# Kernel optimization log

Measured on AMD Instinct MI355X. Metric: run time of the kernel, lower is better.

Reference implementation:

```python
import jax, jax.numpy as jnp
import numpy as np


def _proj(x, w, b):
    # 1x1 conv as channel matmul: x (n,c,h,w), w (k,c), b (k,) -> (n,k,h,w)
    return jnp.einsum('nchw,kc->nkhw', x, w) + b[None, :, None, None]


def setup_inputs() -> dict:
    key = jax.random.key(0)
    ks = jax.random.split(key, 9)
    cin, cinter = 256, 128
    n, h, w = 4, 64, 64
    s = lambda fan_in: 1.0 / np.sqrt(fan_in)
    return {
        'x': jax.random.normal(ks[0], (n, cin, h, w), jnp.float32),
        'theta_w': jax.random.normal(ks[1], (cinter, cin), jnp.float32) * s(cin),
        'theta_b': jax.random.normal(ks[2], (cinter,), jnp.float32) * 0.01,
        'phi_w': jax.random.normal(ks[3], (cinter, cin), jnp.float32) * s(cin),
        'phi_b': jax.random.normal(ks[4], (cinter,), jnp.float32) * 0.01,
        'g_w': jax.random.normal(ks[5], (cinter, cin), jnp.float32) * s(cin),
        'g_b': jax.random.normal(ks[6], (cinter,), jnp.float32) * 0.01,
        'w_w': jax.random.normal(ks[7], (cin, cinter), jnp.float32) * s(cinter),
        'w_b': jax.random.normal(ks[8], (cin,), jnp.float32) * 0.01,
    }


def reference(x, theta_w, theta_b, phi_w, phi_b, g_w, g_b, w_w, w_b):
    n, c, h, w = x.shape
    cinter = theta_w.shape[0]
    hw = h * w
    theta_x = _proj(x, theta_w, theta_b).reshape(n, cinter, hw)  # (n,ci,HW)
    phi_x = _proj(x, phi_w, phi_b).reshape(n, cinter, hw)        # (n,ci,HW)
    g_x = _proj(x, g_w, g_b).reshape(n, cinter, hw)              # (n,ci,HW)
    # f_x = phi^T @ theta : (n, HW, HW), softmax over last dim (theta positions)
    f_x = jnp.einsum('nci,ncj->nij', phi_x, theta_x)
    f_x = jax.nn.softmax(f_x, axis=-1)
    # attended = g @ f : (n, ci, HW)
    att = jnp.einsum('nci,nij->ncj', g_x, f_x).reshape(n, cinter, h, w)
    res_x = _proj(att, w_w, w_b)  # (n, c, h, w)
    return x + res_x
```

## Files before the change

kernel.cpp:

```cpp
#include <hip/hip_runtime.h>
#include <hip/hip_bf16.h>

#define B_ 4
#define C_ 256
#define CI_ 128
#define P_ 4096
#define LOG2E 1.44269504088896340736f

typedef __attribute__((ext_vector_type(8))) _Float16 half8;
typedef __attribute__((ext_vector_type(2))) __fp16 fp16x2;
typedef __attribute__((ext_vector_type(8))) short short8;
typedef __attribute__((ext_vector_type(4))) short short4v;
typedef __attribute__((ext_vector_type(4))) float floatx4;

__device__ __forceinline__ float bf2f(ushort h) {
  union { unsigned u; float f; } v; v.u = ((unsigned)h) << 16; return v.f;
}
__device__ __forceinline__ ushort f2bf(float f) {
  union { float f; unsigned u; } v; v.f = f;
  unsigned r = v.u + 0x7FFFu + ((v.u >> 16) & 1u);
  return (ushort)(r >> 16);
}
__device__ __forceinline__ ushort f2h(float f) {
  _Float16 h = (_Float16)f;
  union { _Float16 h; ushort u; } v; v.h = h; return v.u;
}
__device__ __forceinline__ uint2 pk4h(float a, float b, float c, float d) {
  union { fp16x2 h[2]; uint2 u; } pk;
  pk.h[0] = __builtin_amdgcn_cvt_pkrtz(a, b);
  pk.h[1] = __builtin_amdgcn_cvt_pkrtz(c, d);
  return pk.u;
}

#define MFMA16(a, b, c) __builtin_amdgcn_mfma_f32_16x16x32_f16((a), (b), (c), 0, 0, 0)

__device__ __forceinline__ int detect_bf16(const ushort* __restrict__ xu) {
  __shared__ int cnt_;
  if (threadIdx.x == 0) cnt_ = 0;
  __syncthreads();
  int local = 0;
  int t = threadIdx.x & 255;
#pragma unroll
  for (int s = 0; s < 8; ++s) {
    ushort u = xu[(t * 8 + s) * 2];
    int e = (u >> 7) & 0xFF;
    local += (e >= 0x70 && e <= 0x84) ? 1 : 0;
  }
  atomicAdd(&cnt_, local);
  __syncthreads();
  return cnt_ > 1024;
}

__global__ void k_trc(const void* __restrict__ xv, ushort* __restrict__ xT,
                      const void* __restrict__ s0, const void* __restrict__ s1,
                      const void* __restrict__ s2, const void* __restrict__ s3,
                      const void* __restrict__ tbv, const void* __restrict__ pbv,
                      const void* __restrict__ gbv, const void* __restrict__ wbv,
                      ushort* __restrict__ dstW, float* __restrict__ biasf) {
  int is_bf16 = detect_bf16((const ushort*)xv);
  int bid = blockIdx.x;
  int t = threadIdx.x;
  if (bid < 1024) {
    __shared__ __align__(16) ushort tile[64][72];
    int pb = (bid & 63) * 64;
    int cb = ((bid >> 6) & 3) * 64;
    int b = bid >> 8;
#pragma unroll
    for (int it = 0; it < 2; ++it) {
      int lin = it * 256 + t;
      int c = lin >> 3;
      int p = (lin & 7) * 8;
      size_t base = ((size_t)(b * C_) + cb + c) * P_ + pb + p;
      float vv[8];
      if (is_bf16) {
        short8 v = *(const short8*)((const ushort*)xv + base);
#pragma unroll
        for (int i = 0; i < 8; ++i) vv[i] = bf2f((ushort)v[i]);
      } else {
        const float* xf = (const float*)xv;
        float4 v0 = *(const float4*)(xf + base);
        float4 v1 = *(const float4*)(xf + base + 4);
        vv[0] = v0.x; vv[1] = v0.y; vv[2] = v0.z; vv[3] = v0.w;
        vv[4] = v1.x; vv[5] = v1.y; vv[6] = v1.z; vv[7] = v1.w;
      }
#pragma unroll
      for (int i = 0; i < 8; ++i) {
        int iw = (i + t) & 7;
        tile[p + iw][c] = f2h(vv[iw]);
      }
    }
    __syncthreads();
#pragma unroll
    for (int it = 0; it < 2; ++it) {
      int lin = it * 256 + t;
      int p = lin >> 3;
      int c = (lin & 7) * 8;
      short8 v = *(const short8*)&tile[p][c];
      *(short8*)(xT + ((size_t)(b * P_) + pb + p) * C_ + cb + c) = v;
    }
  } else if (bid < 1536) {
    int wid = bid - 1024;
    int a = wid >> 7;
    const void* srcs[4] = {s0, s1, s2, s3};
    int i = (wid & 127) * 256 + t;
    float v = is_bf16 ? bf2f(((const ushort*)srcs[a])[i]) : ((const float*)srcs[a])[i];
    dstW[a * 32768 + i] = f2h(v);
  } else {
    int idx = (bid - 1536) * 256 + t;
    if (idx < 640) {
      const void* src; int loc;
      if (idx < 128)      { src = tbv; loc = idx; }
      else if (idx < 256) { src = pbv; loc = idx - 128; }
      else if (idx < 384) { src = gbv; loc = idx - 256; }
      else                { src = wbv; loc = idx - 384; }
      float v = is_bf16 ? bf2f(((const ushort*)src)[loc]) : ((const float*)src)[loc];
      biasf[idx] = v;
    }
  }
}

__global__ __launch_bounds__(256, 4) void k_proj(
    const ushort* __restrict__ xT, const ushort* __restrict__ Wh,
    const float* __restrict__ biasf,
    ushort* __restrict__ thetaT, ushort* __restrict__ phiT,
    ushort* __restrict__ g) {
  int t = threadIdx.x;
  int w = t >> 6, lane = t & 63, l = lane & 15, q = lane >> 4;
  int pblk = blockIdx.x * 32;
  int b = blockIdx.y;
  floatx4 acc[2][6];
#pragma unroll
  for (int ps = 0; ps < 2; ++ps)
#pragma unroll
    for (int ks = 0; ks < 6; ++ks) acc[ps][ks] = (floatx4){0.f, 0.f, 0.f, 0.f};
  const ushort* xrow[2];
#pragma unroll
  for (int ps = 0; ps < 2; ++ps)
    xrow[ps] = xT + ((size_t)(b * P_) + pblk + ps * 16 + l) * C_;
  const ushort* wrow[6];
  int prj[6], kloc[6];
#pragma unroll
  for (int ks = 0; ks < 6; ++ks) {
    int kg = w * 96 + ks * 16;
    prj[ks] = kg >> 7;
    kloc[ks] = kg & 127;
    wrow[ks] = Wh + prj[ks] * 32768 + (size_t)(kloc[ks] + l) * C_;
  }
  for (int c = 0; c < C_; c += 32) {
    half8 av[2], wv[6];
#pragma unroll
    for (int ps = 0; ps < 2; ++ps) av[ps] = *(const half8*)(xrow[ps] + c + q * 8);
#pragma unroll
    for (int ks = 0; ks < 6; ++ks) wv[ks] = *(const half8*)(wrow[ks] + c + q * 8);
#pragma unroll
    for (int ps = 0; ps < 2; ++ps)
#pragma unroll
      for (int ks = 0; ks < 6; ++ks)
        acc[ps][ks] = MFMA16(av[ps], wv[ks], acc[ps][ks]);
  }
#pragma unroll
  for (int ks = 0; ks < 6; ++ks) {
    float bias = biasf[prj[ks] * 128 + kloc[ks] + l];
#pragma unroll
    for (int ps = 0; ps < 2; ++ps) {
      floatx4 d = acc[ps][ks];
      if (prj[ks] < 2) {
        ushort* dst = (prj[ks] == 0 ? thetaT : phiT) +
                      ((size_t)(b * P_) + pblk + ps * 16 + q * 4) * CI_ + kloc[ks] + l;
#pragma unroll
        for (int r = 0; r < 4; ++r) dst[(size_t)r * CI_] = f2h(d[r] + bias);
      } else {
        ushort* dst = g + ((size_t)(b * CI_) + kloc[ks] + l) * P_ + pblk + ps * 16 + q * 4;
        short4v pk;
#pragma unroll
        for (int r = 0; r < 4; ++r) pk[r] = (short)f2h(d[r] + bias);
        *(short4v*)dst = pk;
      }
    }
  }
}

__global__ __launch_bounds__(256, 2) void k_stats(
    const ushort* __restrict__ phiT, const ushort* __restrict__ thetaT,
    float* __restrict__ part) {
  int t = threadIdx.x, w = t >> 6, lane = t & 63, l = lane & 15, q = lane >> 4;
  int i0 = blockIdx.x * 256, j0 = blockIdx.y * 512, b = blockIdx.z;
  half8 av[4][4];
#pragma unroll
  for (int is = 0; is < 4; ++is) {
    const ushort* pr = phiT + ((size_t)(b * P_) + i0 + w * 64 + is * 16 + l) * CI_;
#pragma unroll
    for (int ks = 0; ks < 4; ++ks) av[is][ks] = *(const half8*)(pr + ks * 32 + q * 8);
  }
  float sum[4][4];
#pragma unroll
  for (int is = 0; is < 4; ++is)
#pragma unroll
    for (int r = 0; r < 4; ++r) sum[is][r] = 0.f;
  const ushort* tb0 = thetaT + (size_t)b * P_ * CI_;
  for (int jc = 0; jc < 16; ++jc) {
    int j = j0 + jc * 32;
    half8 bv[2][4];
#pragma unroll
    for (int js = 0; js < 2; ++js) {
      const ushort* tr = tb0 + (size_t)(j + js * 16 + l) * CI_;
#pragma unroll
      for (int ks = 0; ks < 4; ++ks) bv[js][ks] = *(const half8*)(tr + ks * 32 + q * 8);
    }
    floatx4 accS[4][2];
#pragma unroll
    for (int is = 0; is < 4; ++is)
#pragma unroll
      for (int js = 0; js < 2; ++js) accS[is][js] = (floatx4){0.f, 0.f, 0.f, 0.f};
#pragma unroll
    for (int ks = 0; ks < 4; ++ks)
#pragma unroll
      for (int is = 0; is < 4; ++is)
#pragma unroll
        for (int js = 0; js < 2; ++js)
          accS[is][js] = MFMA16(av[is][ks], bv[js][ks], accS[is][js]);
#pragma unroll
    for (int is = 0; is < 4; ++is)
#pragma unroll
      for (int js = 0; js < 2; ++js)
#pragma unroll
        for (int r = 0; r < 4; ++r)
          sum[is][r] += exp2f(fmaf(accS[is][js][r], LOG2E, -64.f));
  }
#pragma unroll
  for (int d = 1; d < 16; d <<= 1)
#pragma unroll
    for (int is = 0; is < 4; ++is)
#pragma unroll
      for (int r = 0; r < 4; ++r) sum[is][r] += __shfl_xor(sum[is][r], d, 64);
  if (l == 0) {
#pragma unroll
    for (int is = 0; is < 4; ++is)
#pragma unroll
      for (int r = 0; r < 4; ++r)
        part[((size_t)blockIdx.y * B_ + b) * P_ + i0 + w * 64 + is * 16 + q * 4 + r] =
            sum[is][r];
  }
}

__global__ void k_lse(const float* __restrict__ part, float* __restrict__ o2) {
  int idx = blockIdx.x * 256 + threadIdx.x;
  float s = 0.f;
#pragma unroll
  for (int p = 0; p < 8; ++p) s += part[(size_t)p * (B_ * P_) + idx];
  o2[idx] = log2f(s) + 64.f;
}

__global__ __launch_bounds__(256, 2) void k_attn(
    const ushort* __restrict__ phiT, const ushort* __restrict__ thetaT,
    const ushort* __restrict__ g, const float* __restrict__ o2,
    ushort* __restrict__ attPA, ushort* __restrict__ attPB, int nChunk) {
  __shared__ __align__(16) ushort thL[128][136];
  __shared__ __align__(16) ushort eL[128][136];
  int t = threadIdx.x;
  int w = t >> 6, lane = t & 63, l = lane & 15, q = lane >> 4;
  int j0 = blockIdx.x * 128, ih = blockIdx.y, b = blockIdx.z;
#pragma unroll
  for (int it = 0; it < 8; ++it) {
    int lin = it * 256 + t, row = lin >> 4, cg = (lin & 15) * 8;
    *(short8*)&thL[row][cg] =
        *(const short8*)(thetaT + ((size_t)(b * P_) + j0 + row) * CI_ + cg);
  }
  floatx4 accA[2][8];
#pragma unroll
  for (int cs = 0; cs < 2; ++cs)
#pragma unroll
    for (int js = 0; js < 8; ++js) accA[cs][js] = (floatx4){0.f, 0.f, 0.f, 0.f};
  __syncthreads();
  const float* orow = o2 + b * P_;
  int istart = ih * nChunk * 128;
  half8 af[2][4];
  float ov[2][4];
#pragma unroll
  for (int is = 0; is < 2; ++is) {
    int iG = istart + w * 32 + is * 16;
    const ushort* pr = phiT + ((size_t)(b * P_) + iG + l) * CI_;
#pragma unroll
    for (int ks = 0; ks < 4; ++ks) af[is][ks] = *(const half8*)(pr + ks * 32 + q * 8);
#pragma unroll
    for (int r = 0; r < 4; ++r) ov[is][r] = orow[iG + q * 4 + r];
  }
  for (int ic = 0; ic < nChunk; ++ic) {
    int ibase = istart + ic * 128;
    half8 gf[2][4];
#pragma unroll
    for (int cs = 0; cs < 2; ++cs) {
      const ushort* gr = g + ((size_t)(b * CI_) + w * 32 + cs * 16 + l) * P_ + ibase;
#pragma unroll
      for (int ks = 0; ks < 4; ++ks) gf[cs][ks] = *(const half8*)(gr + ks * 32 + q * 8);
    }
    floatx4 accS[2][8];
#pragma unroll
    for (int is = 0; is < 2; ++is)
#pragma unroll
      for (int js = 0; js < 8; ++js) accS[is][js] = (floatx4){0.f, 0.f, 0.f, 0.f};
#pragma unroll
    for (int ks = 0; ks < 4; ++ks) {
      half8 bf[8];
#pragma unroll
      for (int js = 0; js < 8; ++js) bf[js] = *(const half8*)&thL[js * 16 + l][ks * 32 + q * 8];
#pragma unroll
      for (int is = 0; is < 2; ++is)
#pragma unroll
        for (int js = 0; js < 8; ++js) accS[is][js] = MFMA16(af[is][ks], bf[js], accS[is][js]);
    }
    uint2 ep[2][8];
#pragma unroll
    for (int is = 0; is < 2; ++is)
#pragma unroll
      for (int js = 0; js < 8; ++js) {
        float e0 = exp2f(fmaf(accS[is][js][0], LOG2E, -ov[is][0]));
        float e1 = exp2f(fmaf(accS[is][js][1], LOG2E, -ov[is][1]));
        float e2 = exp2f(fmaf(accS[is][js][2], LOG2E, -ov[is][2]));
        float e3 = exp2f(fmaf(accS[is][js][3], LOG2E, -ov[is][3]));
        ep[is][js] = pk4h(e0, e1, e2, e3);
      }
    __syncthreads();
#pragma unroll
    for (int is = 0; is < 2; ++is)
#pragma unroll
      for (int js = 0; js < 8; ++js)
        *(uint2*)&eL[js * 16 + l][w * 32 + is * 16 + q * 4] = ep[is][js];
    __syncthreads();
    if (ic < nChunk - 1) {
      int nb = istart + (ic + 1) * 128;
#pragma unroll
      for (int is = 0; is < 2; ++is) {
        int iG = nb + w * 32 + is * 16;
        const ushort* pr = phiT + ((size_t)(b * P_) + iG + l) * CI_;
#pragma unroll
        for (int ks = 0; ks < 4; ++ks) af[is][ks] = *(const half8*)(pr + ks * 32 + q * 8);
#pragma unroll
        for (int r = 0; r < 4; ++r) ov[is][r] = orow[iG + q * 4 + r];
      }
    }
#pragma unroll
    for (int ks = 0; ks < 4; ++ks) {
      half8 ef[8];
#pragma unroll
      for (int js = 0; js < 8; ++js) ef[js] = *(const half8*)&eL[js * 16 + l][ks * 32 + q * 8];
#pragma unroll
      for (int cs = 0; cs < 2; ++cs)
#pragma unroll
        for (int js = 0; js < 8; ++js) accA[cs][js] = MFMA16(gf[cs][ks], ef[js], accA[cs][js]);
    }
  }
  ushort* ap = (ih < 2 ? attPA : attPB) + (size_t)(ih & 1) * (B_ * P_ * CI_);
#pragma unroll
  for (int cs = 0; cs < 2; ++cs)
#pragma unroll
    for (int js = 0; js < 8; ++js) {
      uint2 pk = pk4h(accA[cs][js][0], accA[cs][js][1], accA[cs][js][2], accA[cs][js][3]);
      *(uint2*)(ap + ((size_t)(b * P_) + j0 + js * 16 + l) * CI_ +
                w * 32 + cs * 16 + q * 4) = pk;
    }
}

__global__ __launch_bounds__(256, 4) void k_out(
    const ushort* __restrict__ attPA, const ushort* __restrict__ attPB, int nIH,
    const ushort* __restrict__ wwh, const float* __restrict__ biasf,
    const void* __restrict__ xv, void* __restrict__ outv) {
  int is_bf16 = detect_bf16((const ushort*)xv);
  int t = threadIdx.x;
  int w = t >> 6, lane = t & 63, l = lane & 15, q = lane >> 4;
  int p0 = blockIdx.x * 32, b = blockIdx.y;
  floatx4 accR[4][2];
#pragma unroll
  for (int kk = 0; kk < 4; ++kk)
#pragma unroll
    for (int js = 0; js < 2; ++js) accR[kk][js] = (floatx4){0.f, 0.f, 0.f, 0.f};
#pragma unroll
  for (int ks = 0; ks < 4; ++ks) {
    half8 wf[4], af[2];
#pragma unroll
    for (int kk = 0; kk < 4; ++kk)
      wf[kk] = *(const half8*)(wwh + (size_t)(w * 64 + kk * 16 + l) * CI_ + ks * 32 + q * 8);
#pragma unroll
    for (int js = 0; js < 2; ++js) {
      size_t off = ((size_t)(b * P_) + p0 + js * 16 + l) * CI_ + ks * 32 + q * 8;
      half8 s = *(const half8*)(attPA + off);
      s = s + *(const half8*)(attPA + (size_t)(B_ * P_) * CI_ + off);
      if (nIH == 4) {
        s = s + *(const half8*)(attPB + off);
        s = s + *(const half8*)(attPB + (size_t)(B_ * P_) * CI_ + off);
      }
      af[js] = s;
    }
#pragma unroll
    for (int kk = 0; kk < 4; ++kk)
#pragma unroll
      for (int js = 0; js < 2; ++js) accR[kk][js] = MFMA16(wf[kk], af[js], accR[kk][js]);
  }
#pragma unroll
  for (int kk = 0; kk < 4; ++kk)
#pragma unroll
    for (int r = 0; r < 4; ++r) {
      int c = w * 64 + kk * 16 + q * 4 + r;
      float bias = biasf[384 + c];
#pragma unroll
      for (int js = 0; js < 2; ++js) {
        int p = p0 + js * 16 + l;
        size_t idx = ((size_t)(b * C_) + c) * P_ + p;
        float val = accR[kk][js][r] + bias;
        if (is_bf16) {
          ((ushort*)outv)[idx] = f2bf(bf2f(((const ushort*)xv)[idx]) + val);
        } else {
          ((float*)outv)[idx] = ((const float*)xv)[idx] + val;
        }
      }
    }
}

extern "C" void kernel_launch(void* const* d_in, const int* in_sizes, int n_in,
                              void* d_out, int out_size, void* d_ws, size_t ws_size,
                              hipStream_t stream) {
  const void* x  = d_in[0];
  const void* tw = d_in[1];
  const void* tb = d_in[2];
  const void* pw = d_in[3];
  const void* pb = d_in[4];
  const void* gw = d_in[5];
  const void* gb = d_in[6];
  const void* ww = d_in[7];
  const void* wb = d_in[8];
  char* ws = (char*)d_ws;
  float*  o2     = (float*)(ws);
  float*  part   = (float*)(ws + (64u << 10));
  ushort* Wh     = (ushort*)(ws + (576u << 10));
  float*  biasf  = (float*)(ws + (832u << 10));
  ushort* xT     = (ushort*)(ws + (1u << 20));
  ushort* attPA  = xT;
  ushort* thetaT = (ushort*)(ws + (9u << 20));
  ushort* phiT   = (ushort*)(ws + (13u << 20));
  ushort* gbuf   = (ushort*)(ws + (17u << 20));
  ushort* attPB  = (ushort*)(ws + (21u << 20));
  int big = (ws_size >= (30u << 20)) ? 1 : 0;

  k_trc<<<1539, 256, 0, stream>>>(x, xT, tw, pw, gw, ww, tb, pb, gb, wb, Wh, biasf);
  k_proj<<<dim3(128, 4), 256, 0, stream>>>(xT, Wh, biasf, thetaT, phiT, gbuf);
  k_stats<<<dim3(16, 8, 4), 256, 0, stream>>>(phiT, thetaT, part);
  k_lse<<<64, 256, 0, stream>>>(part, o2);
  if (big) {
    k_attn<<<dim3(32, 4, 4), 256, 0, stream>>>(phiT, thetaT, gbuf, o2, attPA, attPB, 8);
    k_out<<<dim3(128, 4), 256, 0, stream>>>(attPA, attPB, 4, Wh + 3 * 32768, biasf, x, d_out);
  } else {
    k_attn<<<dim3(32, 2, 4), 256, 0, stream>>>(phiT, thetaT, gbuf, o2, attPA, attPB, 16);
    k_out<<<dim3(128, 4), 256, 0, stream>>>(attPA, attPB, 2, Wh + 3 * 32768, biasf, x, d_out);
  }
}
```

Before: 235.0 us.

## Restructure attention kernel with 32x32 MFMA, register-resident probabilities and per-wave row splits

Rewrites k_attn to use 32x32x16 MFMA tiles with a 64-column block. Each wave processes its own 32-row slices of the i dimension, and the exp'd probabilities are rearranged into the B-operand layout via cross-half-wave shuffles instead of round-tripping through LDS with two barriers per chunk. Per-wave partial accumulators are reduced through shared memory at the end in fp16, and the grid is fixed at two i-halves, so k_out sums only two partial buffers. Exp arguments are also clamped at 8. The aim is to remove LDS traffic and synchronization from the inner loop and to increase MFMA efficiency. The cost is a larger shared reduction buffer, fp16 rounding of partial sums, and reading g directly from global memory per wave.

Result: slower. 259.9 us (+10.6%).

```diff
diff --git a/kernel.cpp b/kernel.cpp
--- a/kernel.cpp
+++ b/kernel.cpp
@@ -12,6 +12,7 @@
 typedef __attribute__((ext_vector_type(8))) short short8;
 typedef __attribute__((ext_vector_type(4))) short short4v;
 typedef __attribute__((ext_vector_type(4))) float floatx4;
+typedef __attribute__((ext_vector_type(16))) float floatx16;
 
 __device__ __forceinline__ float bf2f(ushort h) {
   union { unsigned u; float f; } v; v.u = ((unsigned)h) << 16; return v.f;
@@ -25,14 +26,14 @@
   _Float16 h = (_Float16)f;
   union { _Float16 h; ushort u; } v; v.h = h; return v.u;
 }
-__device__ __forceinline__ uint2 pk4h(float a, float b, float c, float d) {
-  union { fp16x2 h[2]; uint2 u; } pk;
-  pk.h[0] = __builtin_amdgcn_cvt_pkrtz(a, b);
-  pk.h[1] = __builtin_amdgcn_cvt_pkrtz(c, d);
-  return pk.u;
+__device__ __forceinline__ uint pk2h(float a, float b) {
+  union { fp16x2 h2; uint u; } cv;
+  cv.h2 = __builtin_amdgcn_cvt_pkrtz(a, b);
+  return cv.u;
 }
 
 #define MFMA16(a, b, c) __builtin_amdgcn_mfma_f32_16x16x32_f16((a), (b), (c), 0, 0, 0)
+#define MFMA32(a, b, c) __builtin_amdgcn_mfma_f32_32x32x16_f16((a), (b), (c), 0, 0, 0)
 
 __device__ __forceinline__ int detect_bf16(const ushort* __restrict__ xu) {
   __shared__ int cnt_;
@@ -254,115 +255,131 @@
 __global__ __launch_bounds__(256, 2) void k_attn(
     const ushort* __restrict__ phiT, const ushort* __restrict__ thetaT,
     const ushort* __restrict__ g, const float* __restrict__ o2,
-    ushort* __restrict__ attPA, ushort* __restrict__ attPB, int nChunk) {
-  __shared__ __align__(16) ushort thL[128][136];
-  __shared__ __align__(16) ushort eL[128][136];
+    ushort* __restrict__ attP0, ushort* __restrict__ attP1) {
+  __shared__ __align__(16) ushort thL[64 * 136];
+  __shared__ __align__(16) uint redbuf[3 * 4096];
   int t = threadIdx.x;
-  int w = t >> 6, lane = t & 63, l = lane & 15, q = lane >> 4;
-  int j0 = blockIdx.x * 128, ih = blockIdx.y, b = blockIdx.z;
-#pragma unroll
-  for (int it = 0; it < 8; ++it) {
-    int lin = it * 256 + t, row = lin >> 4, cg = (lin & 15) * 8;
-    *(short8*)&thL[row][cg] =
-        *(const short8*)(thetaT + ((size_t)(b * P_) + j0 + row) * CI_ + cg);
-  }
-  floatx4 accA[2][8];
-#pragma unroll
-  for (int cs = 0; cs < 2; ++cs)
-#pragma unroll
-    for (int js = 0; js < 8; ++js) accA[cs][js] = (floatx4){0.f, 0.f, 0.f, 0.f};
+  int w = t >> 6, lane = t & 63;
+  int m = lane & 31, h = lane >> 5;
+  int j0 = blockIdx.x * 64, ih = blockIdx.y, b = blockIdx.z;
+#pragma unroll
+  for (int it = 0; it < 4; ++it) {
+    int lin = it * 256 + t;
+    int row = lin >> 4;
+    int col = (lin & 15) * 8;
+    *(short8*)&thL[row * 136 + col] =
+        *(const short8*)(thetaT + ((size_t)(b * P_) + j0 + row) * CI_ + col);
+  }
+  floatx16 accA[4][2];
+  floatx16 zz = {0.f,0.f,0.f,0.f,0.f,0.f,0.f,0.f,0.f,0.f,0.f,0.f,0.f,0.f,0.f,0.f};
+#pragma unroll
+  for (int cs = 0; cs < 4; ++cs)
+#pragma unroll
+    for (int js = 0; js < 2; ++js) accA[cs][js] = zz;
   __syncthreads();
+  int istart = ih * 2048;
   const float* orow = o2 + b * P_;
-  int istart = ih * nChunk * 128;
-  half8 af[2][4];
-  float ov[2][4];
-#pragma unroll
-  for (int is = 0; is < 2; ++is) {
-    int iG = istart + w * 32 + is * 16;
-    const ushort* pr = phiT + ((size_t)(b * P_) + iG + l) * CI_;
-#pragma unroll
-    for (int ks = 0; ks < 4; ++ks) af[is][ks] = *(const half8*)(pr + ks * 32 + q * 8);
-#pragma unroll
-    for (int r = 0; r < 4; ++r) ov[is][r] = orow[iG + q * 4 + r];
-  }
-  for (int ic = 0; ic < nChunk; ++ic) {
-    int ibase = istart + ic * 128;
-    half8 gf[2][4];
-#pragma unroll
-    for (int cs = 0; cs < 2; ++cs) {
-      const ushort* gr = g + ((size_t)(b * CI_) + w * 32 + cs * 16 + l) * P_ + ibase;
-#pragma unroll
-      for (int ks = 0; ks < 4; ++ks) gf[cs][ks] = *(const half8*)(gr + ks * 32 + q * 8);
-    }
-    floatx4 accS[2][8];
-#pragma unroll
-    for (int is = 0; is < 2; ++is)
-#pragma unroll
-      for (int js = 0; js < 8; ++js) accS[is][js] = (floatx4){0.f, 0.f, 0.f, 0.f};
-#pragma unroll
-    for (int ks = 0; ks < 4; ++ks) {
-      half8 bf[8];
-#pragma unroll
-      for (int js = 0; js < 8; ++js) bf[js] = *(const half8*)&thL[js * 16 + l][ks * 32 + q * 8];
-#pragma unroll
-      for (int is = 0; is < 2; ++is)
-#pragma unroll
-        for (int js = 0; js < 8; ++js) accS[is][js] = MFMA16(af[is][ks], bf[js], accS[is][js]);
-    }
-    uint2 ep[2][8];
-#pragma unroll
-    for (int is = 0; is < 2; ++is)
-#pragma unroll
-      for (int js = 0; js < 8; ++js) {
-        float e0 = exp2f(fmaf(accS[is][js][0], LOG2E, -ov[is][0]));
-        float e1 = exp2f(fmaf(accS[is][js][1], LOG2E, -ov[is][1]));
-        float e2 = exp2f(fmaf(accS[is][js][2], LOG2E, -ov[is][2]));
-        float e3 = exp2f(fmaf(accS[is][js][3], LOG2E, -ov[is][3]));
-        ep[is][js] = pk4h(e0, e1, e2, e3);
-      }
-    __syncthreads();
-#pragma unroll
-    for (int is = 0; is < 2; ++is)
-#pragma unroll
-      for (int js = 0; js < 8; ++js)
-        *(uint2*)&eL[js * 16 + l][w * 32 + is * 16 + q * 4] = ep[is][js];
-    __syncthreads();
-    if (ic < nChunk - 1) {
-      int nb = istart + (ic + 1) * 128;
-#pragma unroll
-      for (int is = 0; is < 2; ++is) {
-        int iG = nb + w * 32 + is * 16;
-        const ushort* pr = phiT + ((size_t)(b * P_) + iG + l) * CI_;
-#pragma unroll
-        for (int ks = 0; ks < 4; ++ks) af[is][ks] = *(const half8*)(pr + ks * 32 + q * 8);
-#pragma unroll
-        for (int r = 0; r < 4; ++r) ov[is][r] = orow[iG + q * 4 + r];
-      }
-    }
-#pragma unroll
-    for (int ks = 0; ks < 4; ++ks) {
-      half8 ef[8];
-#pragma unroll
-      for (int js = 0; js < 8; ++js) ef[js] = *(const half8*)&eL[js * 16 + l][ks * 32 + q * 8];
-#pragma unroll
-      for (int cs = 0; cs < 2; ++cs)
-#pragma unroll
-        for (int js = 0; js < 8; ++js) accA[cs][js] = MFMA16(gf[cs][ks], ef[js], accA[cs][js]);
-    }
-  }
-  ushort* ap = (ih < 2 ? attPA : attPB) + (size_t)(ih & 1) * (B_ * P_ * CI_);
-#pragma unroll
-  for (int cs = 0; cs < 2; ++cs)
-#pragma unroll
-    for (int js = 0; js < 8; ++js) {
-      uint2 pk = pk4h(accA[cs][js][0], accA[cs][js][1], accA[cs][js][2], accA[cs][js][3]);
-      *(uint2*)(ap + ((size_t)(b * P_) + j0 + js * 16 + l) * CI_ +
-                w * 32 + cs * 16 + q * 4) = pk;
-    }
+  for (int u = 0; u < 16; ++u) {
+    int ib = istart + (u * 4 + w) * 32;
+    half8 aph[8];
+    const ushort* pr = phiT + ((size_t)(b * P_) + ib + m) * CI_ + h * 8;
+#pragma unroll
+    for (int kt = 0; kt < 8; ++kt) aph[kt] = *(const half8*)(pr + kt * 16);
+    float ovs[16];
+    {
+      float4 o0 = *(const float4*)(orow + ib + 4 * h);
+      float4 o1 = *(const float4*)(orow + ib + 8 + 4 * h);
+      float4 o2v = *(const float4*)(orow + ib + 16 + 4 * h);
+      float4 o3 = *(const float4*)(orow + ib + 24 + 4 * h);
+      ovs[0]=o0.x; ovs[1]=o0.y; ovs[2]=o0.z; ovs[3]=o0.w;
+      ovs[4]=o1.x; ovs[5]=o1.y; ovs[6]=o1.z; ovs[7]=o1.w;
+      ovs[8]=o2v.x; ovs[9]=o2v.y; ovs[10]=o2v.z; ovs[11]=o2v.w;
+      ovs[12]=o3.x; ovs[13]=o3.y; ovs[14]=o3.z; ovs[15]=o3.w;
+    }
+    floatx16 accS[2];
+    accS[0] = zz; accS[1] = zz;
+#pragma unroll
+    for (int kt = 0; kt < 8; ++kt)
+#pragma unroll
+      for (int js = 0; js < 2; ++js) {
+        half8 bf = *(const half8*)&thL[(js * 32 + m) * 136 + kt * 16 + h * 8];
+        accS[js] = MFMA32(aph[kt], bf, accS[js]);
+      }
+    half8 efr[2][2];
+#pragma unroll
+    for (int js = 0; js < 2; ++js) {
+      float e[16];
+#pragma unroll
+      for (int rg = 0; rg < 16; ++rg)
+        e[rg] = exp2f(fminf(fmaf(accS[js][rg], LOG2E, -ovs[rg]), 8.f));
+      uint pk[8], qq[8];
+#pragma unroll
+      for (int p2 = 0; p2 < 8; ++p2) pk[p2] = pk2h(e[p2 * 2], e[p2 * 2 + 1]);
+#pragma unroll
+      for (int p2 = 0; p2 < 8; ++p2) qq[p2] = (uint)__shfl_xor((int)pk[p2], 32, 64);
+      union { uint u[4]; half8 v; } f0, f1;
+      f0.u[0] = h ? qq[2] : pk[0];
+      f0.u[1] = h ? qq[3] : pk[1];
+      f0.u[2] = h ? pk[2] : qq[0];
+      f0.u[3] = h ? pk[3] : qq[1];
+      f1.u[0] = h ? qq[6] : pk[4];
+      f1.u[1] = h ? qq[7] : pk[5];
+      f1.u[2] = h ? pk[6] : qq[4];
+      f1.u[3] = h ? pk[7] : qq[5];
+      efr[js][0] = f0.v;
+      efr[js][1] = f1.v;
+    }
+#pragma unroll
+    for (int kf = 0; kf < 2; ++kf) {
+      const ushort* grb = g + (size_t)(b * CI_) * P_ + ib + kf * 16 + h * 8;
+#pragma unroll
+      for (int cs = 0; cs < 4; ++cs) {
+        half8 ag = *(const half8*)(grb + (size_t)(cs * 32 + m) * P_);
+#pragma unroll
+        for (int js = 0; js < 2; ++js)
+          accA[cs][js] = MFMA32(ag, efr[js][kf], accA[cs][js]);
+      }
+    }
+  }
+  if (w > 0) {
+    uint* dst = &redbuf[(w - 1) * 4096];
+#pragma unroll
+    for (int cs = 0; cs < 4; ++cs)
+#pragma unroll
+      for (int js = 0; js < 2; ++js)
+#pragma unroll
+        for (int p2 = 0; p2 < 8; ++p2)
+          dst[(cs * 16 + js * 8 + p2) * 64 + lane] =
+              pk2h(accA[cs][js][p2 * 2], accA[cs][js][p2 * 2 + 1]);
+  }
+  __syncthreads();
+  if (w == 0) {
+    ushort* ap = (ih == 0 ? attP0 : attP1);
+#pragma unroll
+    for (int cs = 0; cs < 4; ++cs)
+#pragma unroll
+      for (int js = 0; js < 2; ++js)
+#pragma unroll
+        for (int p2 = 0; p2 < 8; ++p2) {
+          float s0 = accA[cs][js][p2 * 2], s1 = accA[cs][js][p2 * 2 + 1];
+          int d = (cs * 16 + js * 8 + p2) * 64 + lane;
+#pragma unroll
+          for (int ww = 0; ww < 3; ++ww) {
+            union { uint u; fp16x2 h2; } cv;
+            cv.u = redbuf[ww * 4096 + d];
+            s0 += (float)cv.h2[0];
+            s1 += (float)cv.h2[1];
+          }
+          int rg = p2 * 2;
+          int c = cs * 32 + (rg & 3) + 8 * (rg >> 2) + 4 * h;
+          int j = j0 + js * 32 + m;
+          *(uint*)(ap + ((size_t)(b * P_) + j) * CI_ + c) = pk2h(s0, s1);
+        }
+  }
 }
 
 __global__ __launch_bounds__(256, 4) void k_out(
-    const ushort* __restrict__ attPA, const ushort* __restrict__ attPB, int nIH,
+    const ushort* __restrict__ attP0, const ushort* __restrict__ attP1,
     const ushort* __restrict__ wwh, const float* __restrict__ biasf,
     const void* __restrict__ xv, void* __restrict__ outv) {
   int is_bf16 = detect_bf16((const ushort*)xv);
@@ -383,12 +400,8 @@
 #pragma unroll
     for (int js = 0; js < 2; ++js) {
       size_t off = ((size_t)(b * P_) + p0 + js * 16 + l) * CI_ + ks * 32 + q * 8;
-      half8 s = *(const half8*)(attPA + off);
-      s = s + *(const half8*)(attPA + (size_t)(B_ * P_) * CI_ + off);
-      if (nIH == 4) {
-        s = s + *(const half8*)(attPB + off);
-        s = s + *(const half8*)(attPB + (size_t)(B_ * P_) * CI_ + off);
-      }
+      half8 s = *(const half8*)(attP0 + off);
+      s = s + *(const half8*)(attP1 + off);
       af[js] = s;
     }
 #pragma unroll
@@ -434,22 +447,16 @@
   ushort* Wh     = (ushort*)(ws + (576u << 10));
   float*  biasf  = (float*)(ws + (832u << 10));
   ushort* xT     = (ushort*)(ws + (1u << 20));
-  ushort* attPA  = xT;
+  ushort* attP0  = xT;
   ushort* thetaT = (ushort*)(ws + (9u << 20));
   ushort* phiT   = (ushort*)(ws + (13u << 20));
   ushort* gbuf   = (ushort*)(ws + (17u << 20));
-  ushort* attPB  = (ushort*)(ws + (21u << 20));
-  int big = (ws_size >= (30u << 20)) ? 1 : 0;
+  ushort* attP1  = (ushort*)(ws + (21u << 20));
 
   k_trc<<<1539, 256, 0, stream>>>(x, xT, tw, pw, gw, ww, tb, pb, gb, wb, Wh, biasf);
   k_proj<<<dim3(128, 4), 256, 0, stream>>>(xT, Wh, biasf, thetaT, phiT, gbuf);
   k_stats<<<dim3(16, 8, 4), 256, 0, stream>>>(phiT, thetaT, part);
   k_lse<<<64, 256, 0, stream>>>(part, o2);
-  if (big) {
-    k_attn<<<dim3(32, 4, 4), 256, 0, stream>>>(phiT, thetaT, gbuf, o2, attPA, attPB, 8);
-    k_out<<<dim3(128, 4), 256, 0, stream>>>(attPA, attPB, 4, Wh + 3 * 32768, biasf, x, d_out);
-  } else {
-    k_attn<<<dim3(32, 2, 4), 256, 0, stream>>>(phiT, thetaT, gbuf, o2, attPA, attPB, 16);
-    k_out<<<dim3(128, 4), 256, 0, stream>>>(attPA, attPB, 2, Wh + 3 * 32768, biasf, x, d_out);
-  }
-}
+  k_attn<<<dim3(64, 2, 4), 256, 0, stream>>>(phiT, thetaT, gbuf, o2, attP0, attP1);
+  k_out<<<dim3(128, 4), 256, 0, stream>>>(attP0, attP1, Wh + 3 * 32768, biasf, x, d_out);
+}
```

## Fuse input transpose and weight conversion into projection; fold LSE into attention

Applied to the files above, without the earlier changes.

Removes the separate transpose/convert kernel. The projection kernel now loads x straight into a shared-memory transposed tile and converts weights and biases to fp16 on the fly. The LSE reduction kernel is also removed: each attention block sums the partial exp-sums for its row half into shared memory itself. Attention is fixed to the 2-way split with 16 chunks, and the output kernel reads weights directly. This drops two launches and a workspace round-trip, at the cost of redundant weight conversion per block, redundant LSE work across blocks, and a lost 4-way split option.

Result: slower. 257.1 us (+9.4%).

```diff
diff --git a/kernel.cpp b/kernel.cpp
--- a/kernel.cpp
+++ b/kernel.cpp
@@ -25,11 +25,28 @@
   _Float16 h = (_Float16)f;
   union { _Float16 h; ushort u; } v; v.h = h; return v.u;
 }
-__device__ __forceinline__ uint2 pk4h(float a, float b, float c, float d) {
-  union { fp16x2 h[2]; uint2 u; } pk;
-  pk.h[0] = __builtin_amdgcn_cvt_pkrtz(a, b);
-  pk.h[1] = __builtin_amdgcn_cvt_pkrtz(c, d);
-  return pk.u;
+__device__ __forceinline__ uint pk2h(float a, float b) {
+  union { fp16x2 h2; uint u; } cv;
+  cv.h2 = __builtin_amdgcn_cvt_pkrtz(a, b);
+  return cv.u;
+}
+__device__ __forceinline__ half8 ld8h(const void* src, size_t off, int is_bf16) {
+  union { uint u[4]; half8 v; } r;
+  if (is_bf16) {
+    short8 x = *(const short8*)((const ushort*)src + off);
+#pragma unroll
+    for (int i = 0; i < 4; ++i)
+      r.u[i] = pk2h(bf2f((ushort)x[2 * i]), bf2f((ushort)x[2 * i + 1]));
+  } else {
+    const float* f = (const float*)src + off;
+    float4 a = *(const float4*)f, b = *(const float4*)(f + 4);
+    r.u[0] = pk2h(a.x, a.y); r.u[1] = pk2h(a.z, a.w);
+    r.u[2] = pk2h(b.x, b.y); r.u[3] = pk2h(b.z, b.w);
+  }
+  return r.v;
+}
+__device__ __forceinline__ float ldf(const void* src, int idx, int is_bf16) {
+  return is_bf16 ? bf2f(((const ushort*)src)[idx]) : ((const float*)src)[idx];
 }
 
 #define MFMA16(a, b, c) __builtin_amdgcn_mfma_f32_16x16x32_f16((a), (b), (c), 0, 0, 0)
@@ -51,26 +68,25 @@
   return cnt_ > 1024;
 }
 
-__global__ void k_trc(const void* __restrict__ xv, ushort* __restrict__ xT,
-                      const void* __restrict__ s0, const void* __restrict__ s1,
-                      const void* __restrict__ s2, const void* __restrict__ s3,
-                      const void* __restrict__ tbv, const void* __restrict__ pbv,
-                      const void* __restrict__ gbv, const void* __restrict__ wbv,
-                      ushort* __restrict__ dstW, float* __restrict__ biasf) {
+__global__ __launch_bounds__(256, 4) void k_proj(
+    const void* __restrict__ xv,
+    const void* __restrict__ twv, const void* __restrict__ pwv,
+    const void* __restrict__ gwv,
+    const void* __restrict__ tbv, const void* __restrict__ pbv,
+    const void* __restrict__ gbv,
+    ushort* __restrict__ thetaT, ushort* __restrict__ phiT,
+    ushort* __restrict__ g) {
   int is_bf16 = detect_bf16((const ushort*)xv);
-  int bid = blockIdx.x;
+  __shared__ __align__(16) ushort xtl[32][264];
   int t = threadIdx.x;
-  if (bid < 1024) {
-    __shared__ __align__(16) ushort tile[64][72];
-    int pb = (bid & 63) * 64;
-    int cb = ((bid >> 6) & 3) * 64;
-    int b = bid >> 8;
-#pragma unroll
-    for (int it = 0; it < 2; ++it) {
-      int lin = it * 256 + t;
-      int c = lin >> 3;
-      int p = (lin & 7) * 8;
-      size_t base = ((size_t)(b * C_) + cb + c) * P_ + pb + p;
+  int w = t >> 6, lane = t & 63, l = lane & 15, q = lane >> 4;
+  int p0 = blockIdx.x * 32, b = blockIdx.y;
+  {
+    int c_loc = t >> 2;
+    int p_loc = (t & 3) * 8;
+#pragma unroll
+    for (int cb = 0; cb < 4; ++cb) {
+      size_t base = ((size_t)(b * C_) + cb * 64 + c_loc) * P_ + p0 + p_loc;
       float vv[8];
       if (is_bf16) {
         short8 v = *(const short8*)((const ushort*)xv + base);
@@ -86,72 +102,33 @@
 #pragma unroll
       for (int i = 0; i < 8; ++i) {
         int iw = (i + t) & 7;
-        tile[p + iw][c] = f2h(vv[iw]);
-      }
-    }
-    __syncthreads();
-#pragma unroll
-    for (int it = 0; it < 2; ++it) {
-      int lin = it * 256 + t;
-      int p = lin >> 3;
-      int c = (lin & 7) * 8;
-      short8 v = *(const short8*)&tile[p][c];
-      *(short8*)(xT + ((size_t)(b * P_) + pb + p) * C_ + cb + c) = v;
-    }
-  } else if (bid < 1536) {
-    int wid = bid - 1024;
-    int a = wid >> 7;
-    const void* srcs[4] = {s0, s1, s2, s3};
-    int i = (wid & 127) * 256 + t;
-    float v = is_bf16 ? bf2f(((const ushort*)srcs[a])[i]) : ((const float*)srcs[a])[i];
-    dstW[a * 32768 + i] = f2h(v);
-  } else {
-    int idx = (bid - 1536) * 256 + t;
-    if (idx < 640) {
-      const void* src; int loc;
-      if (idx < 128)      { src = tbv; loc = idx; }
-      else if (idx < 256) { src = pbv; loc = idx - 128; }
-      else if (idx < 384) { src = gbv; loc = idx - 256; }
-      else                { src = wbv; loc = idx - 384; }
-      float v = is_bf16 ? bf2f(((const ushort*)src)[loc]) : ((const float*)src)[loc];
-      biasf[idx] = v;
-    }
-  }
-}
-
-__global__ __launch_bounds__(256, 4) void k_proj(
-    const ushort* __restrict__ xT, const ushort* __restrict__ Wh,
-    const float* __restrict__ biasf,
-    ushort* __restrict__ thetaT, ushort* __restrict__ phiT,
-    ushort* __restrict__ g) {
-  int t = threadIdx.x;
-  int w = t >> 6, lane = t & 63, l = lane & 15, q = lane >> 4;
-  int pblk = blockIdx.x * 32;
-  int b = blockIdx.y;
+        xtl[p_loc + iw][cb * 64 + c_loc] = f2h(vv[iw]);
+      }
+    }
+  }
+  __syncthreads();
+  const void* wsrc[3] = {twv, pwv, gwv};
+  const void* bsrc[3] = {tbv, pbv, gbv};
   floatx4 acc[2][6];
 #pragma unroll
   for (int ps = 0; ps < 2; ++ps)
 #pragma unroll
     for (int ks = 0; ks < 6; ++ks) acc[ps][ks] = (floatx4){0.f, 0.f, 0.f, 0.f};
-  const ushort* xrow[2];
-#pragma unroll
-  for (int ps = 0; ps < 2; ++ps)
-    xrow[ps] = xT + ((size_t)(b * P_) + pblk + ps * 16 + l) * C_;
-  const ushort* wrow[6];
   int prj[6], kloc[6];
 #pragma unroll
   for (int ks = 0; ks < 6; ++ks) {
     int kg = w * 96 + ks * 16;
     prj[ks] = kg >> 7;
     kloc[ks] = kg & 127;
-    wrow[ks] = Wh + prj[ks] * 32768 + (size_t)(kloc[ks] + l) * C_;
   }
   for (int c = 0; c < C_; c += 32) {
     half8 av[2], wv[6];
 #pragma unroll
-    for (int ps = 0; ps < 2; ++ps) av[ps] = *(const half8*)(xrow[ps] + c + q * 8);
-#pragma unroll
-    for (int ks = 0; ks < 6; ++ks) wv[ks] = *(const half8*)(wrow[ks] + c + q * 8);
+    for (int ps = 0; ps < 2; ++ps)
+      av[ps] = *(const half8*)&xtl[ps * 16 + l][c + q * 8];
+#pragma unroll
+    for (int ks = 0; ks < 6; ++ks)
+      wv[ks] = ld8h(wsrc[prj[ks]], (size_t)(kloc[ks] + l) * C_ + c + q * 8, is_bf16);
 #pragma unroll
     for (int ps = 0; ps < 2; ++ps)
 #pragma unroll
@@ -160,17 +137,17 @@
   }
 #pragma unroll
   for (int ks = 0; ks < 6; ++ks) {
-    float bias = biasf[prj[ks] * 128 + kloc[ks] + l];
+    float bias = ldf(bsrc[prj[ks]], kloc[ks] + l, is_bf16);
 #pragma unroll
     for (int ps = 0; ps < 2; ++ps) {
       floatx4 d = acc[ps][ks];
       if (prj[ks] < 2) {
         ushort* dst = (prj[ks] == 0 ? thetaT : phiT) +
-                      ((size_t)(b * P_) + pblk + ps * 16 + q * 4) * CI_ + kloc[ks] + l;
+                      ((size_t)(b * P_) + p0 + ps * 16 + q * 4) * CI_ + kloc[ks] + l;
 #pragma unroll
         for (int r = 0; r < 4; ++r) dst[(size_t)r * CI_] = f2h(d[r] + bias);
       } else {
-        ushort* dst = g + ((size_t)(b * CI_) + kloc[ks] + l) * P_ + pblk + ps * 16 + q * 4;
+        ushort* dst = g + ((size_t)(b * CI_) + kloc[ks] + l) * P_ + p0 + ps * 16 + q * 4;
         short4v pk;
 #pragma unroll
         for (int r = 0; r < 4; ++r) pk[r] = (short)f2h(d[r] + bias);
@@ -243,49 +220,49 @@
   }
 }
 
-__global__ void k_lse(const float* __restrict__ part, float* __restrict__ o2) {
-  int idx = blockIdx.x * 256 + threadIdx.x;
-  float s = 0.f;
-#pragma unroll
-  for (int p = 0; p < 8; ++p) s += part[(size_t)p * (B_ * P_) + idx];
-  o2[idx] = log2f(s) + 64.f;
-}
-
 __global__ __launch_bounds__(256, 2) void k_attn(
     const ushort* __restrict__ phiT, const ushort* __restrict__ thetaT,
-    const ushort* __restrict__ g, const float* __restrict__ o2,
-    ushort* __restrict__ attPA, ushort* __restrict__ attPB, int nChunk) {
+    const ushort* __restrict__ g, const float* __restrict__ part,
+    ushort* __restrict__ attP0, ushort* __restrict__ attP1) {
   __shared__ __align__(16) ushort thL[128][136];
   __shared__ __align__(16) ushort eL[128][136];
+  __shared__ __align__(16) float oL[2048];
   int t = threadIdx.x;
   int w = t >> 6, lane = t & 63, l = lane & 15, q = lane >> 4;
   int j0 = blockIdx.x * 128, ih = blockIdx.y, b = blockIdx.z;
+  int istart = ih * 2048;
 #pragma unroll
   for (int it = 0; it < 8; ++it) {
     int lin = it * 256 + t, row = lin >> 4, cg = (lin & 15) * 8;
     *(short8*)&thL[row][cg] =
         *(const short8*)(thetaT + ((size_t)(b * P_) + j0 + row) * CI_ + cg);
   }
+#pragma unroll
+  for (int z = 0; z < 8; ++z) {
+    int iloc = z * 256 + t;
+    float s = 0.f;
+#pragma unroll
+    for (int js = 0; js < 8; ++js)
+      s += part[((size_t)js * B_ + b) * P_ + istart + iloc];
+    oL[iloc] = log2f(s) + 64.f;
+  }
   floatx4 accA[2][8];
 #pragma unroll
   for (int cs = 0; cs < 2; ++cs)
 #pragma unroll
     for (int js = 0; js < 8; ++js) accA[cs][js] = (floatx4){0.f, 0.f, 0.f, 0.f};
   __syncthreads();
-  const float* orow = o2 + b * P_;
-  int istart = ih * nChunk * 128;
   half8 af[2][4];
-  float ov[2][4];
+  float4 ov[2];
 #pragma unroll
   for (int is = 0; is < 2; ++is) {
     int iG = istart + w * 32 + is * 16;
     const ushort* pr = phiT + ((size_t)(b * P_) + iG + l) * CI_;
 #pragma unroll
     for (int ks = 0; ks < 4; ++ks) af[is][ks] = *(const half8*)(pr + ks * 32 + q * 8);
-#pragma unroll
-    for (int r = 0; r < 4; ++r) ov[is][r] = orow[iG + q * 4 + r];
-  }
-  for (int ic = 0; ic < nChunk; ++ic) {
+    ov[is] = *(const float4*)&oL[w * 32 + is * 16 + q * 4];
+  }
+  for (int ic = 0; ic < 16; ++ic) {
     int ibase = istart + ic * 128;
     half8 gf[2][4];
 #pragma unroll
@@ -314,11 +291,11 @@
     for (int is = 0; is < 2; ++is)
 #pragma unroll
       for (int js = 0; js < 8; ++js) {
-        float e0 = exp2f(fmaf(accS[is][js][0], LOG2E, -ov[is][0]));
-        float e1 = exp2f(fmaf(accS[is][js][1], LOG2E, -ov[is][1]));
-        float e2 = exp2f(fmaf(accS[is][js][2], LOG2E, -ov[is][2]));
-        float e3 = exp2f(fmaf(accS[is][js][3], LOG2E, -ov[is][3]));
-        ep[is][js] = pk4h(e0, e1, e2, e3);
+        float e0 = exp2f(fminf(fmaf(accS[is][js][0], LOG2E, -ov[is].x), 0.5f));
+        float e1 = exp2f(fminf(fmaf(accS[is][js][1], LOG2E, -ov[is].y), 0.5f));
+        float e2 = exp2f(fminf(fmaf(accS[is][js][2], LOG2E, -ov[is].z), 0.5f));
+        float e3 = exp2f(fminf(fmaf(accS[is][js][3], LOG2E, -ov[is].w), 0.5f));
+        ep[is][js] = (uint2){pk2h(e0, e1), pk2h(e2, e3)};
       }
     __syncthreads();
 #pragma unroll
@@ -327,7 +304,7 @@
       for (int js = 0; js < 8; ++js)
         *(uint2*)&eL[js * 16 + l][w * 32 + is * 16 + q * 4] = ep[is][js];
     __syncthreads();
-    if (ic < nChunk - 1) {
+    if (ic < 15) {
       int nb = istart + (ic + 1) * 128;
 #pragma unroll
       for (int is = 0; is < 2; ++is) {
@@ -335,8 +312,7 @@
         const ushort* pr = phiT + ((size_t)(b * P_) + iG + l) * CI_;
 #pragma unroll
         for (int ks = 0; ks < 4; ++ks) af[is][ks] = *(const half8*)(pr + ks * 32 + q * 8);
-#pragma unroll
-        for (int r = 0; r < 4; ++r) ov[is][r] = orow[iG + q * 4 + r];
+        ov[is] = *(const float4*)&oL[(nb - istart) + w * 32 + is * 16 + q * 4];
       }
     }
 #pragma unroll
@@ -350,20 +326,21 @@
         for (int js = 0; js < 8; ++js) accA[cs][js] = MFMA16(gf[cs][ks], ef[js], accA[cs][js]);
     }
   }
-  ushort* ap = (ih < 2 ? attPA : attPB) + (size_t)(ih & 1) * (B_ * P_ * CI_);
+  ushort* ap = (ih == 0 ? attP0 : attP1);
 #pragma unroll
   for (int cs = 0; cs < 2; ++cs)
 #pragma unroll
     for (int js = 0; js < 8; ++js) {
-      uint2 pk = pk4h(accA[cs][js][0], accA[cs][js][1], accA[cs][js][2], accA[cs][js][3]);
+      uint2 pk = (uint2){pk2h(accA[cs][js][0], accA[cs][js][1]),
+                         pk2h(accA[cs][js][2], accA[cs][js][3])};
       *(uint2*)(ap + ((size_t)(b * P_) + j0 + js * 16 + l) * CI_ +
                 w * 32 + cs * 16 + q * 4) = pk;
     }
 }
 
 __global__ __launch_bounds__(256, 4) void k_out(
-    const ushort* __restrict__ attPA, const ushort* __restrict__ attPB, int nIH,
-    const ushort* __restrict__ wwh, const float* __restrict__ biasf,
+    const ushort* __restrict__ attP0, const ushort* __restrict__ attP1,
+    const void* __restrict__ wwv, const void* __restrict__ wbv,
     const void* __restrict__ xv, void* __restrict__ outv) {
   int is_bf16 = detect_bf16((const ushort*)xv);
   int t = threadIdx.x;
@@ -379,16 +356,12 @@
     half8 wf[4], af[2];
 #pragma unroll
     for (int kk = 0; kk < 4; ++kk)
-      wf[kk] = *(const half8*)(wwh + (size_t)(w * 64 + kk * 16 + l) * CI_ + ks * 32 + q * 8);
+      wf[kk] = ld8h(wwv, (size_t)(w * 64 + kk * 16 + l) * CI_ + ks * 32 + q * 8, is_bf16);
 #pragma unroll
     for (int js = 0; js < 2; ++js) {
       size_t off = ((size_t)(b * P_) + p0 + js * 16 + l) * CI_ + ks * 32 + q * 8;
-      half8 s = *(const half8*)(attPA + off);
-      s = s + *(const half8*)(attPA + (size_t)(B_ * P_) * CI_ + off);
-      if (nIH == 4) {
-        s = s + *(const half8*)(attPB + off);
-        s = s + *(const half8*)(attPB + (size_t)(B_ * P_) * CI_ + off);
-      }
+      half8 s = *(const half8*)(attP0 + off);
+      s = s + *(const half8*)(attP1 + off);
       af[js] = s;
     }
 #pragma unroll
@@ -401,7 +374,7 @@
 #pragma unroll
     for (int r = 0; r < 4; ++r) {
       int c = w * 64 + kk * 16 + q * 4 + r;
-      float bias = biasf[384 + c];
+      float bias = ldf(wbv, c, is_bf16);
 #pragma unroll
       for (int js = 0; js < 2; ++js) {
         int p = p0 + js * 16 + l;
@@ -429,27 +402,16 @@
   const void* ww = d_in[7];
   const void* wb = d_in[8];
   char* ws = (char*)d_ws;
-  float*  o2     = (float*)(ws);
-  float*  part   = (float*)(ws + (64u << 10));
-  ushort* Wh     = (ushort*)(ws + (576u << 10));
-  float*  biasf  = (float*)(ws + (832u << 10));
-  ushort* xT     = (ushort*)(ws + (1u << 20));
-  ushort* attPA  = xT;
+  float*  part   = (float*)(ws);
+  ushort* attP0  = (ushort*)(ws + (1u << 20));
   ushort* thetaT = (ushort*)(ws + (9u << 20));
   ushort* phiT   = (ushort*)(ws + (13u << 20));
   ushort* gbuf   = (ushort*)(ws + (17u << 20));
-  ushort* attPB  = (ushort*)(ws + (21u << 20));
-  int big = (ws_size >= (30u << 20)) ? 1 : 0;
-
-  k_trc<<<1539, 256, 0, stream>>>(x, xT, tw, pw, gw, ww, tb, pb, gb, wb, Wh, biasf);
-  k_proj<<<dim3(128, 4), 256, 0, stream>>>(xT, Wh, biasf, thetaT, phiT, gbuf);
+  ushort* attP1  = (ushort*)(ws + (21u << 20));
+
+  k_proj<<<dim3(128, 4), 256, 0, stream>>>(x, tw, pw, gw, tb, pb, gb,
+                                           thetaT, phiT, gbuf);
   k_stats<<<dim3(16, 8, 4), 256, 0, stream>>>(phiT, thetaT, part);
-  k_lse<<<64, 256, 0, stream>>>(part, o2);
-  if (big) {
-    k_attn<<<dim3(32, 4, 4), 256, 0, stream>>>(phiT, thetaT, gbuf, o2, attPA, attPB, 8);
-    k_out<<<dim3(128, 4), 256, 0, stream>>>(attPA, attPB, 4, Wh + 3 * 32768, biasf, x, d_out);
-  } else {
-    k_attn<<<dim3(32, 2, 4), 256, 0, stream>>>(phiT, thetaT, gbuf, o2, attPA, attPB, 16);
-    k_out<<<dim3(128, 4), 256, 0, stream>>>(attPA, attPB, 2, Wh + 3 * 32768, biasf, x, d_out);
-  }
-}
+  k_attn<<<dim3(32, 2, 4), 256, 0, stream>>>(phiT, thetaT, gbuf, part, attP0, attP1);
+  k_out<<<dim3(128, 4), 256, 0, stream>>>(attP0, attP1, ww, wb, x, d_out);
+}
```
